# Performance work log

Hardware: AMD Instinct MI355X
Metric: run time of the kernel (lower is better)

## Reference

```python
import jax, jax.numpy as jnp
import numpy as np

B, T, C = 2, 2048, 2048
N_HEAD, N_KV_HEAD, HEAD_DIM = 16, 4, 128
N_REP = N_HEAD // N_KV_HEAD
EPS = 1e-05


def setup_inputs() -> dict:
    key = jax.random.key(0)
    ks = jax.random.split(key, 8)
    # rope freqs as cos/sin of theta_t,i = t / 10000^(2i/d)
    inv_freq = 1.0 / (10000.0 ** (np.arange(0, HEAD_DIM, 2, dtype=np.float32) / HEAD_DIM))
    ang = np.arange(T, dtype=np.float32)[:, None] * inv_freq[None, :]  # [T, HEAD_DIM//2]
    scale = 0.02
    return {
        "x": jax.random.normal(ks[0], (B, T, C), jnp.float32),
        "freqs_cos": jnp.asarray(np.cos(ang)),
        "freqs_sin": jnp.asarray(np.sin(ang)),
        "wq": jax.random.normal(ks[1], (C, N_HEAD * HEAD_DIM), jnp.float32) * scale,
        "wk": jax.random.normal(ks[2], (C, N_KV_HEAD * HEAD_DIM), jnp.float32) * scale,
        "wv": jax.random.normal(ks[3], (C, N_KV_HEAD * HEAD_DIM), jnp.float32) * scale,
        "wo": jax.random.normal(ks[4], (N_HEAD * HEAD_DIM, C), jnp.float32) * scale,
        "q_norm_w": jnp.ones((HEAD_DIM,), jnp.float32),
        "k_norm_w": jnp.ones((HEAD_DIM,), jnp.float32),
    }


def _rmsnorm(x, w):
    var = jnp.mean(jnp.square(x), axis=-1, keepdims=True)
    return x * jax.lax.rsqrt(var + EPS) * w


def _rope(x, cos, sin):
    # x: [B, T, H, D]; interpret last dim as interleaved (real, imag) pairs
    xr = x[..., 0::2]
    xi = x[..., 1::2]
    c = cos[None, :, None, :]
    s = sin[None, :, None, :]
    out_r = xr * c - xi * s
    out_i = xr * s + xi * c
    return jnp.stack([out_r, out_i], axis=-1).reshape(x.shape)


def reference(x, freqs_cos, freqs_sin, wq, wk, wv, wo, q_norm_w, k_norm_w):
    # QKV projections
    xq = (x @ wq).reshape(B, T, N_HEAD, HEAD_DIM)
    xk = (x @ wk).reshape(B, T, N_KV_HEAD, HEAD_DIM)
    xv = (x @ wv).reshape(B, T, N_KV_HEAD, HEAD_DIM)
    # optional q/k RMSNorm (use_qk_norm=True)
    xq = _rmsnorm(xq, q_norm_w)
    xk = _rmsnorm(xk, k_norm_w)
    # RoPE
    xq = _rope(xq, freqs_cos, freqs_sin)
    xk = _rope(xk, freqs_cos, freqs_sin)
    # GQA expand: each kv head repeated N_REP times contiguously
    xk = jnp.repeat(xk, N_REP, axis=2)  # [B, T, N_HEAD, D]
    xv = jnp.repeat(xv, N_REP, axis=2)
    # causal SDPA
    scores = jnp.einsum("bthd,bshd->bhts", xq, xk) / jnp.sqrt(jnp.float32(HEAD_DIM))
    causal = jnp.tril(jnp.ones((T, T), bool))
    scores = jnp.where(causal[None, None], scores, jnp.float32(-1e30))
    attn = jax.nn.softmax(scores, axis=-1)
    y = jnp.einsum("bhts,bshd->bthd", attn, xv).reshape(B, T, N_HEAD * HEAD_DIM)
    return y @ wo
```

## Files before the change

### kernel.cpp

```cpp
#include <hip/hip_runtime.h>
#include <hip/hip_bf16.h>

using u16 = unsigned short;
using u32 = unsigned int;

typedef short bf16x8 __attribute__((ext_vector_type(8)));
typedef float f32x4 __attribute__((ext_vector_type(4)));

#define AS1 __attribute__((address_space(1)))
#define AS3 __attribute__((address_space(3)))

__device__ __forceinline__ void gll16(const void* g, void* l) {
  __builtin_amdgcn_global_load_lds((const AS1 u32*)g, (AS3 u32*)l, 16, 0, 0);
}

__device__ __forceinline__ u16 f2bf(float x) {
  u32 u = __builtin_bit_cast(u32, x);
  u32 r = (u + 0x7fffu + ((u >> 16) & 1u)) >> 16;
  return (u16)r;
}
__device__ __forceinline__ u32 pk2(float lo, float hi) {
  return (u32)f2bf(lo) | ((u32)f2bf(hi) << 16);
}
__device__ __forceinline__ u16 f2bf_fast(float x) {
  __hip_bfloat16 h = __float2bfloat16(x);
  return __builtin_bit_cast(u16, h);
}

__device__ __forceinline__ void trans64(const float* __restrict__ in, u16* __restrict__ out,
                                        int R, int Cc, int bx, int by, float (*tl)[65]) {
  int c0 = bx * 64, r0 = by * 64, tid = threadIdx.x;
#pragma unroll
  for (int i = 0; i < 16; i++) {
    int idx = i * 256 + tid; int tr = idx >> 6, tc = idx & 63;
    tl[tr][tc] = in[(size_t)(r0 + tr) * Cc + c0 + tc];
  }
  __syncthreads();
#pragma unroll
  for (int i = 0; i < 16; i++) {
    int idx = i * 256 + tid; int tr = idx >> 6, tc = idx & 63;
    out[(size_t)(c0 + tr) * R + r0 + tc] = f2bf(tl[tc][tr]);
  }
}

__global__ void k_prep(const float* __restrict__ x, u16* __restrict__ xb,
                       const float* __restrict__ wq, u16* __restrict__ wqt,
                       const float* __restrict__ wk, const float* __restrict__ wv,
                       u16* __restrict__ wkvt,
                       const float* __restrict__ wo, u16* __restrict__ wot,
                       const float* __restrict__ fc, const float* __restrict__ fs,
                       float2* __restrict__ fcs) {
  __shared__ float tl[64][65];
  int gid = blockIdx.x;
  if (gid < 4096) {
    int i = gid * 256 + threadIdx.x;
    const float4* p = (const float4*)(x + (size_t)i * 8);
    float4 a = p[0], b = p[1];
    uint4 o;
    o.x = pk2(a.x, a.y); o.y = pk2(a.z, a.w);
    o.z = pk2(b.x, b.y); o.w = pk2(b.z, b.w);
    *(uint4*)(xb + (size_t)i * 8) = o;
  } else if (gid < 5120) {
    int t = gid - 4096; trans64(wq, wqt, 2048, 2048, t & 31, t >> 5, tl);
  } else if (gid < 5376) {
    int t = gid - 5120; trans64(wk, wkvt, 2048, 512, t & 7, t >> 3, tl);
  } else if (gid < 5632) {
    int t = gid - 5376; trans64(wv, wkvt + 512 * 2048, 2048, 512, t & 7, t >> 3, tl);
  } else if (gid < 6656) {
    int t = gid - 5632; trans64(wo, wot, 2048, 2048, t & 31, t >> 5, tl);
  } else {
    int base = (gid - 6656) * 2048 + threadIdx.x * 8;
#pragma unroll
    for (int j = 0; j < 8; j++) {
      int idx = base + j;
      fcs[idx] = make_float2(fc[idx], fs[idx]);
    }
  }
}

template <int MODE>
__global__ __launch_bounds__(256) void k_gemm(
    const u16* __restrict__ A, const u16* __restrict__ BT0, const u16* __restrict__ BT1,
    void* __restrict__ Cout, u16* __restrict__ Kout, u16* __restrict__ Vout, int K,
    const float* __restrict__ nwq, const float* __restrict__ nwk,
    const float2* __restrict__ fcs) {
  constexpr int NX = (MODE == 0) ? 16 : 24;
  constexpr int RBX = (MODE == 0) ? 8 : 12;
  __shared__ char lds[32768];
  char* As = lds; char* Bs = lds + 16384;
  int tid = threadIdx.x, w = tid >> 6, l = tid & 63, lg = l >> 4, ll = l & 15;
  int lid = blockIdx.y * NX + blockIdx.x;
  int xcd = lid & 7, r = lid >> 3;
  int colg = xcd & 1, rowg = xcd >> 1;
  int bxt = colg * RBX + r % RBX;
  int bm0 = (rowg * 8 + r / RBX) * 128;
  bool qpath = (MODE == 0) || (bxt < 16);
  const u16* BT = qpath ? BT0 : BT1;
  int bn0 = qpath ? bxt * 128 : (bxt - 16) * 128;
  int wr = w >> 1, wc = w & 1;
  f32x4 acc[4][4] = {};
  for (int k0 = 0; k0 < K; k0 += 64) {
#pragma unroll
    for (int i = 0; i < 4; i++) {
      int base = i * 256 + (w << 6);
      int p = base + l;
      int rr = p >> 3, kc = (p & 7) ^ (rr & 7);
      gll16(A + (size_t)(bm0 + rr) * K + k0 + kc * 8, As + base * 16);
      gll16(BT + (size_t)(bn0 + rr) * K + k0 + kc * 8, Bs + base * 16);
    }
    asm volatile("s_waitcnt vmcnt(0)" ::: "memory");
    __syncthreads();
#pragma unroll
    for (int ks = 0; ks < 2; ks++) {
      bf16x8 af[4], bfr[4];
#pragma unroll
      for (int m = 0; m < 4; m++) {
        int row = 64 * wr + 16 * m + ll;
        af[m] = *(const bf16x8*)(As + row * 128 + (((lg + 4 * ks) ^ (row & 7)) << 4));
      }
#pragma unroll
      for (int n = 0; n < 4; n++) {
        int row = 64 * wc + 16 * n + ll;
        bfr[n] = *(const bf16x8*)(Bs + row * 128 + (((lg + 4 * ks) ^ (row & 7)) << 4));
      }
#pragma unroll
      for (int m = 0; m < 4; m++)
#pragma unroll
        for (int n = 0; n < 4; n++)
          acc[m][n] = __builtin_amdgcn_mfma_f32_16x16x32_bf16(af[m], bfr[n], acc[m][n], 0, 0, 0);
    }
    __syncthreads();
  }

  if (MODE == 0) {
    float* C = (float*)Cout;
#pragma unroll
    for (int m = 0; m < 4; m++)
#pragma unroll
      for (int n = 0; n < 4; n++) {
        int row = bm0 + 64 * wr + 16 * m + 4 * lg;
        int col = bn0 + 64 * wc + 16 * n + ll;
        float* cp = C + (size_t)row * 2048 + col;
#pragma unroll
        for (int r2 = 0; r2 < 4; r2++) cp[(size_t)r2 * 2048] = acc[m][n][r2];
      }
    return;
  }

  if (qpath || bn0 < 512) {
    const float* nw = qpath ? nwq : nwk;
    u16* O = qpath ? (u16*)Cout : Kout;
    int ostride = qpath ? 2048 : 512;
    float outscale = qpath ? 0.12751744843f : 1.0f;
    float* ssum = (float*)lds;
    float ps[4][4];
#pragma unroll
    for (int m = 0; m < 4; m++)
#pragma unroll
      for (int r2 = 0; r2 < 4; r2++) {
        float p = 0.f;
#pragma unroll
        for (int n = 0; n < 4; n++) p += acc[m][n][r2] * acc[m][n][r2];
#pragma unroll
        for (int msk = 1; msk < 16; msk <<= 1) p += __shfl_xor(p, msk);
        ps[m][r2] = p;
      }
    if (ll == 0) {
#pragma unroll
      for (int m = 0; m < 4; m++)
#pragma unroll
        for (int r2 = 0; r2 < 4; r2++)
          ssum[wr * 128 + (16 * m + 4 * lg + r2) * 2 + wc] = ps[m][r2];
    }
    __syncthreads();
    float rs[4][4];
#pragma unroll
    for (int m = 0; m < 4; m++)
#pragma unroll
      for (int r2 = 0; r2 < 4; r2++) {
        int rowl = 16 * m + 4 * lg + r2;
        float tot = ssum[wr * 128 + rowl * 2] + ssum[wr * 128 + rowl * 2 + 1];
        rs[m][r2] = rsqrtf(tot * (1.0f / 128.0f) + 1e-5f) * outscale;
      }
#pragma unroll
    for (int m = 0; m < 4; m++)
#pragma unroll
      for (int n = 0; n < 4; n++) {
        int d = 64 * wc + 16 * n + ll;
        float wgt = nw[d];
        int i = d >> 1;
#pragma unroll
        for (int r2 = 0; r2 < 4; r2++) {
          int row = bm0 + 64 * wr + 16 * m + 4 * lg + r2;
          int t = row & 2047;
          float y = acc[m][n][r2] * rs[m][r2] * wgt;
          float p = __shfl_xor(y, 1);
          float2 cs = fcs[t * 64 + i];
          float o = (ll & 1) ? (p * cs.y + y * cs.x) : (y * cs.x - p * cs.y);
          O[(size_t)row * ostride + bn0 + d] = f2bf(o);
        }
      }
  } else {
    int b = bm0 >> 11, t0g = bm0 & 2047;
    int kvh = (bn0 - 512) >> 7;
    int bk = b * 4 + kvh;
#pragma unroll
    for (int m = 0; m < 4; m++)
#pragma unroll
      for (int n = 0; n < 4; n++) {
        int d = 64 * wc + 16 * n + ll;
        int tloc = 64 * wr + 16 * m + 4 * lg;
        u32 w0 = pk2(acc[m][n][0], acc[m][n][1]);
        u32 w1 = pk2(acc[m][n][2], acc[m][n][3]);
        int byte = (d * 256 + tloc * 2) ^ ((d & 7) << 4);
        *(uint2*)(lds + byte) = make_uint2(w0, w1);
      }
    __syncthreads();
    int tc = tid & 15, dbase = tid >> 4;
#pragma unroll
    for (int pass = 0; pass < 8; pass++) {
      int d = dbase + pass * 16;
      int byte = (d * 256 + tc * 16) ^ ((d & 7) << 4);
      uint4 v = *(const uint4*)(lds + byte);
      *(uint4*)(Vout + ((size_t)(bk * 128 + d)) * 2048 + t0g + tc * 8) = v;
    }
  }
}

__global__ __launch_bounds__(256, 4) void k_attn(
    const u16* __restrict__ Q, const u16* __restrict__ Kb,
    const u16* __restrict__ Vt, u16* __restrict__ Y) {
  __shared__ char lds[73728];
  char* Ps = lds + 65536;
  int tid = threadIdx.x, w = tid >> 6, l = tid & 63, lg = l >> 4, ll = l & 15;
  int fid = blockIdx.x;
  int g = fid & 7, rank = fid >> 3;
  int b = g >> 2, kvh = g & 3;
  int h = kvh * 4 + (rank & 3);
  int pairId = rank >> 2;
  const u16* Kbase = Kb + ((size_t)b * 2048) * 512 + kvh * 128;
  const u16* Vbase = Vt + ((size_t)(b * 4 + kvh) * 128) * 2048;

  const bf16x8 vones = {(short)0x3F80, (short)0x3F80, (short)0x3F80, (short)0x3F80,
                        (short)0x3F80, (short)0x3F80, (short)0x3F80, (short)0x3F80};

#pragma unroll 1
  for (int qi = 0; qi < 2; qi++) {
    int qb = qi ? (31 - pairId) : pairId;
    int q0 = qb * 64;
    bf16x8 qf[4];
    {
      int qrow = b * 2048 + q0 + 16 * w + ll;
      const u16* qp = Q + (size_t)qrow * 2048 + h * 128;
#pragma unroll
      for (int ks = 0; ks < 4; ks++) qf[ks] = *(const bf16x8*)(qp + ks * 32 + lg * 8);
    }
    f32x4 o[8] = {};
    f32x4 lacc = {};

    auto stage = [&](int bi, int k0) {
      char* Kd = lds + (bi ? 32768 : 0);
      char* Vd = lds + (bi ? 49152 : 16384);
#pragma unroll
      for (int i = 0; i < 4; i++) {
        int c = i * 256 + tid;
        int dst = (i * 256 + (w << 6)) * 16;
        int krow = c >> 4, ksrc = (c & 15) ^ (krow & 7);
        gll16(Kbase + (size_t)(k0 + krow) * 512 + ksrc * 8, Kd + dst);
        int vd = c >> 3, vsrc = (c & 7) ^ (vd & 7);
        gll16(Vbase + (size_t)vd * 2048 + k0 + vsrc * 8, Vd + dst);
      }
    };

    stage(0, 0);
    asm volatile("s_waitcnt vmcnt(0)" ::: "memory");
    __syncthreads();

    int cur = 0;
    for (int it = 0; it <= qb; ++it) {
      if (it < qb) stage(cur ^ 1, (it + 1) * 64);
      char* Ks = lds + (cur ? 32768 : 0);
      char* Vs = lds + (cur ? 49152 : 16384);
      f32x4 s[4] = {};
      __builtin_amdgcn_s_setprio(1);
#pragma unroll
      for (int ks = 0; ks < 4; ks++) {
#pragma unroll
        for (int n = 0; n < 4; n++) {
          int row = 16 * n + ll;
          bf16x8 kf = *(const bf16x8*)(Ks + ((row * 256 + (lg + 4 * ks) * 16) ^ ((row & 7) << 4)));
          s[n] = __builtin_amdgcn_mfma_f32_16x16x32_bf16(qf[ks], kf, s[n], 0, 0, 0);
        }
      }
      __builtin_amdgcn_s_setprio(0);
      if (it == qb) {
        int k0 = it * 64;
#pragma unroll
        for (int n = 0; n < 4; n++) {
          int kk = k0 + 16 * n + ll;
#pragma unroll
          for (int r = 0; r < 4; r++) {
            int qq = q0 + 16 * w + 4 * lg + r;
            if (kk > qq) s[n][r] = -1e30f;
          }
        }
      }
#pragma unroll
      for (int r = 0; r < 4; r++) {
        int prow = 4 * lg + r;
#pragma unroll
        for (int n = 0; n < 4; n++) {
          float e = exp2f(s[n][r]);
          int byte = (w << 11) + ((prow * 128 + (16 * n + ll) * 2) ^ ((prow & 7) << 4));
          *(u16*)(Ps + byte) = f2bf_fast(e);
        }
      }
      __builtin_amdgcn_s_setprio(1);
#pragma unroll
      for (int ks = 0; ks < 2; ks++) {
        bf16x8 pf = *(const bf16x8*)(Ps + (w << 11) + ((ll * 128 + (lg + 4 * ks) * 16) ^ ((ll & 7) << 4)));
        lacc = __builtin_amdgcn_mfma_f32_16x16x32_bf16(pf, vones, lacc, 0, 0, 0);
#pragma unroll
        for (int n = 0; n < 8; n++) {
          int row = 16 * n + ll;
          bf16x8 vf = *(const bf16x8*)(Vs + ((row * 128 + (lg + 4 * ks) * 16) ^ ((row & 7) << 4)));
          o[n] = __builtin_amdgcn_mfma_f32_16x16x32_bf16(pf, vf, o[n], 0, 0, 0);
        }
      }
      __builtin_amdgcn_s_setprio(0);
      asm volatile("s_waitcnt vmcnt(0)" ::: "memory");
      __syncthreads();
      cur ^= 1;
    }
    float rl[4];
#pragma unroll
    for (int r = 0; r < 4; r++) rl[r] = 1.0f / lacc[r];
#pragma unroll
    for (int n = 0; n < 8; n++) {
      int col = h * 128 + 16 * n + ll;
#pragma unroll
      for (int r = 0; r < 4; r++) {
        int trow = b * 2048 + q0 + 16 * w + 4 * lg + r;
        Y[(size_t)trow * 2048 + col] = f2bf_fast(o[n][r] * rl[r]);
      }
    }
  }
  (void)Vbase;
}

extern "C" void kernel_launch(void* const* d_in, const int* in_sizes, int n_in,
                              void* d_out, int out_size, void* d_ws, size_t ws_size,
                              hipStream_t stream) {
  const float* x   = (const float*)d_in[0];
  const float* fc  = (const float*)d_in[1];
  const float* fs  = (const float*)d_in[2];
  const float* wq  = (const float*)d_in[3];
  const float* wk  = (const float*)d_in[4];
  const float* wv  = (const float*)d_in[5];
  const float* wo  = (const float*)d_in[6];
  const float* qnw = (const float*)d_in[7];
  const float* knw = (const float*)d_in[8];
  float* out = (float*)d_out;

  const size_t MB = 1ull << 20;
  char* ws = (char*)d_ws;
  u16*    xb   = (u16*)(ws);
  u16*    wqt  = (u16*)(ws + 16 * MB);
  u16*    wkvt = (u16*)(ws + 24 * MB);
  u16*    wot  = (u16*)(ws + 28 * MB);
  u16*    Qb   = (u16*)(ws + 36 * MB);
  u16*    Kbq  = (u16*)(ws + 52 * MB);
  u16*    Vtg  = (u16*)(ws + 56 * MB);
  u16*    Yb   = (u16*)(ws + 60 * MB);
  float2* fcs  = (float2*)(ws + 76 * MB);

  hipLaunchKernelGGL(k_prep, dim3(6720), dim3(256), 0, stream,
                     x, xb, wq, wqt, wk, wv, wkvt, wo, wot, fc, fs, fcs);
  hipLaunchKernelGGL((k_gemm<3>), dim3(24, 32), dim3(256), 0, stream,
                     xb, wqt, wkvt, (void*)Qb, Kbq, Vtg, 2048,
                     qnw, knw, fcs);
  hipLaunchKernelGGL(k_attn, dim3(512), dim3(256), 0, stream, Qb, Kbq, Vtg, Yb);
  hipLaunchKernelGGL((k_gemm<0>), dim3(16, 32), dim3(256), 0, stream,
                     Yb, wot, (const u16*)nullptr, (void*)out, (u16*)nullptr, (u16*)nullptr, 2048,
                     nullptr, nullptr, nullptr);
}
```

Before: 216.0 us.

## Split QKV GEMM into triple-buffered 512-thread kernel with prefetch pipeline

```diff
diff --git a/kernel.cpp b/kernel.cpp
--- a/kernel.cpp
+++ b/kernel.cpp
@@ -84,8 +84,8 @@
     void* __restrict__ Cout, u16* __restrict__ Kout, u16* __restrict__ Vout, int K,
     const float* __restrict__ nwq, const float* __restrict__ nwk,
     const float2* __restrict__ fcs) {
-  constexpr int NX = (MODE == 0) ? 16 : 24;
-  constexpr int RBX = (MODE == 0) ? 8 : 12;
+  constexpr int NX = 16;
+  constexpr int RBX = 8;
   __shared__ char lds[32768];
   char* As = lds; char* Bs = lds + 16384;
   int tid = threadIdx.x, w = tid >> 6, l = tid & 63, lg = l >> 4, ll = l & 15;
@@ -94,9 +94,8 @@
   int colg = xcd & 1, rowg = xcd >> 1;
   int bxt = colg * RBX + r % RBX;
   int bm0 = (rowg * 8 + r / RBX) * 128;
-  bool qpath = (MODE == 0) || (bxt < 16);
-  const u16* BT = qpath ? BT0 : BT1;
-  int bn0 = qpath ? bxt * 128 : (bxt - 16) * 128;
+  const u16* BT = BT0;
+  int bn0 = bxt * 128;
   int wr = w >> 1, wc = w & 1;
   f32x4 acc[4][4] = {};
   for (int k0 = 0; k0 < K; k0 += 64) {
@@ -131,25 +130,96 @@
     }
     __syncthreads();
   }
-
-  if (MODE == 0) {
-    float* C = (float*)Cout;
-#pragma unroll
-    for (int m = 0; m < 4; m++)
-#pragma unroll
-      for (int n = 0; n < 4; n++) {
-        int row = bm0 + 64 * wr + 16 * m + 4 * lg;
-        int col = bn0 + 64 * wc + 16 * n + ll;
-        float* cp = C + (size_t)row * 2048 + col;
-#pragma unroll
-        for (int r2 = 0; r2 < 4; r2++) cp[(size_t)r2 * 2048] = acc[m][n][r2];
-      }
-    return;
+  float* C = (float*)Cout;
+#pragma unroll
+  for (int m = 0; m < 4; m++)
+#pragma unroll
+    for (int n = 0; n < 4; n++) {
+      int row = bm0 + 64 * wr + 16 * m + 4 * lg;
+      int col = bn0 + 64 * wc + 16 * n + ll;
+      float* cp = C + (size_t)row * 2048 + col;
+#pragma unroll
+      for (int r2 = 0; r2 < 4; r2++) cp[(size_t)r2 * 2048] = acc[m][n][r2];
+    }
+  (void)nwq; (void)nwk; (void)fcs; (void)Kout; (void)Vout;
+}
+
+__global__ __launch_bounds__(512, 2) void k_gemm_qkv(
+    const u16* __restrict__ A, const u16* __restrict__ BT0, const u16* __restrict__ BT1,
+    u16* __restrict__ Qout, u16* __restrict__ Kout, u16* __restrict__ Vout,
+    const float* __restrict__ nwq, const float* __restrict__ nwk,
+    const float2* __restrict__ fcs) {
+  __shared__ char lds[98304];
+  const int K = 2048;
+  int tid = threadIdx.x, w = tid >> 6, l = tid & 63, lg = l >> 4, ll = l & 15;
+  int wr = w >> 2, wc = w & 3;
+  int lid = blockIdx.y * 24 + blockIdx.x;
+  int xcd = lid & 7, r = lid >> 3;
+  int colg = xcd & 1, rowg = xcd >> 1;
+  int bxt = colg * 12 + r % 12;
+  int bm0 = (rowg * 8 + r / 12) * 128;
+  bool qpath = (bxt < 16);
+  const u16* BT = qpath ? BT0 : BT1;
+  int bn0 = qpath ? bxt * 128 : (bxt - 16) * 128;
+
+  auto stage = [&](int si, int kt) {
+    char* Sb = lds + si * 32768;
+    int k0 = kt * 64;
+#pragma unroll
+    for (int i = 0; i < 2; i++) {
+      int base = i * 512 + (w << 6) + ((tid >> 8) << 8);
+      base = i * 512 + (w << 6);
+      int c = base + l;
+      int row = c >> 3, kc = (c & 7) ^ (row & 7);
+      gll16(A + (size_t)(bm0 + row) * K + k0 + kc * 8, Sb + base * 16);
+      gll16(BT + (size_t)(bn0 + row) * K + k0 + kc * 8, Sb + 16384 + base * 16);
+    }
+  };
+
+  f32x4 acc[4][2] = {};
+  stage(0, 0); stage(1, 1);
+  asm volatile("s_waitcnt vmcnt(4)" ::: "memory");
+  __builtin_amdgcn_s_barrier();
+  __builtin_amdgcn_sched_barrier(0);
+
+  for (int kt = 0; kt < 32; ++kt) {
+    int cs = kt % 3;
+    if (kt + 2 < 32) stage((kt + 2) % 3, kt + 2);
+    char* As = lds + cs * 32768;
+    char* Bs = As + 16384;
+    __builtin_amdgcn_s_setprio(1);
+#pragma unroll
+    for (int ks = 0; ks < 2; ks++) {
+      bf16x8 af[4], bf[2];
+#pragma unroll
+      for (int m = 0; m < 4; m++) {
+        int row = 64 * wr + 16 * m + ll;
+        af[m] = *(const bf16x8*)(As + row * 128 + (((lg + 4 * ks) ^ (row & 7)) << 4));
+      }
+#pragma unroll
+      for (int n = 0; n < 2; n++) {
+        int row = 32 * wc + 16 * n + ll;
+        bf[n] = *(const bf16x8*)(Bs + row * 128 + (((lg + 4 * ks) ^ (row & 7)) << 4));
+      }
+#pragma unroll
+      for (int m = 0; m < 4; m++)
+#pragma unroll
+        for (int n = 0; n < 2; n++)
+          acc[m][n] = __builtin_amdgcn_mfma_f32_16x16x32_bf16(af[m], bf[n], acc[m][n], 0, 0, 0);
+    }
+    __builtin_amdgcn_s_setprio(0);
+    if (kt + 2 < 32) {
+      asm volatile("s_waitcnt vmcnt(4)" ::: "memory");
+    } else {
+      asm volatile("s_waitcnt vmcnt(0)" ::: "memory");
+    }
+    __builtin_amdgcn_s_barrier();
+    __builtin_amdgcn_sched_barrier(0);
   }
 
   if (qpath || bn0 < 512) {
     const float* nw = qpath ? nwq : nwk;
-    u16* O = qpath ? (u16*)Cout : Kout;
+    u16* O = qpath ? Qout : Kout;
     int ostride = qpath ? 2048 : 512;
     float outscale = qpath ? 0.12751744843f : 1.0f;
     float* ssum = (float*)lds;
@@ -160,7 +230,7 @@
       for (int r2 = 0; r2 < 4; r2++) {
         float p = 0.f;
 #pragma unroll
-        for (int n = 0; n < 4; n++) p += acc[m][n][r2] * acc[m][n][r2];
+        for (int n = 0; n < 2; n++) p += acc[m][n][r2] * acc[m][n][r2];
 #pragma unroll
         for (int msk = 1; msk < 16; msk <<= 1) p += __shfl_xor(p, msk);
         ps[m][r2] = p;
@@ -170,7 +240,7 @@
       for (int m = 0; m < 4; m++)
 #pragma unroll
         for (int r2 = 0; r2 < 4; r2++)
-          ssum[wr * 128 + (16 * m + 4 * lg + r2) * 2 + wc] = ps[m][r2];
+          ssum[wr * 256 + (16 * m + 4 * lg + r2) * 4 + wc] = ps[m][r2];
     }
     __syncthreads();
     float rs[4][4];
@@ -179,14 +249,16 @@
 #pragma unroll
       for (int r2 = 0; r2 < 4; r2++) {
         int rowl = 16 * m + 4 * lg + r2;
-        float tot = ssum[wr * 128 + rowl * 2] + ssum[wr * 128 + rowl * 2 + 1];
+        const float* sp = ssum + wr * 256 + rowl * 4;
+        float tot = sp[0] + sp[1] + sp[2] + sp[3];
         rs[m][r2] = rsqrtf(tot * (1.0f / 128.0f) + 1e-5f) * outscale;
       }
 #pragma unroll
     for (int m = 0; m < 4; m++)
 #pragma unroll
-      for (int n = 0; n < 4; n++) {
-        int d = 64 * wc + 16 * n + ll;
+      for (int n = 0; n < 2; n++) {
+        int col = bn0 + 32 * wc + 16 * n + ll;
+        int d = col & 127;
         float wgt = nw[d];
         int i = d >> 1;
 #pragma unroll
@@ -197,7 +269,7 @@
           float p = __shfl_xor(y, 1);
           float2 cs = fcs[t * 64 + i];
           float o = (ll & 1) ? (p * cs.y + y * cs.x) : (y * cs.x - p * cs.y);
-          O[(size_t)row * ostride + bn0 + d] = f2bf(o);
+          O[(size_t)row * ostride + col] = f2bf(o);
         }
       }
   } else {
@@ -207,8 +279,8 @@
 #pragma unroll
     for (int m = 0; m < 4; m++)
 #pragma unroll
-      for (int n = 0; n < 4; n++) {
-        int d = 64 * wc + 16 * n + ll;
+      for (int n = 0; n < 2; n++) {
+        int d = 32 * wc + 16 * n + ll;
         int tloc = 64 * wr + 16 * m + 4 * lg;
         u32 w0 = pk2(acc[m][n][0], acc[m][n][1]);
         u32 w1 = pk2(acc[m][n][2], acc[m][n][3]);
@@ -218,8 +290,8 @@
     __syncthreads();
     int tc = tid & 15, dbase = tid >> 4;
 #pragma unroll
-    for (int pass = 0; pass < 8; pass++) {
-      int d = dbase + pass * 16;
+    for (int pass = 0; pass < 4; pass++) {
+      int d = dbase + pass * 32;
       int byte = (d * 256 + tc * 16) ^ ((d & 7) << 4);
       uint4 v = *(const uint4*)(lds + byte);
       *(uint4*)(Vout + ((size_t)(bk * 128 + d)) * 2048 + t0g + tc * 8) = v;
@@ -376,9 +448,8 @@
 
   hipLaunchKernelGGL(k_prep, dim3(6720), dim3(256), 0, stream,
                      x, xb, wq, wqt, wk, wv, wkvt, wo, wot, fc, fs, fcs);
-  hipLaunchKernelGGL((k_gemm<3>), dim3(24, 32), dim3(256), 0, stream,
-                     xb, wqt, wkvt, (void*)Qb, Kbq, Vtg, 2048,
-                     qnw, knw, fcs);
+  hipLaunchKernelGGL(k_gemm_qkv, dim3(24, 32), dim3(512), 0, stream,
+                     xb, wqt, wkvt, Qb, Kbq, Vtg, qnw, knw, fcs);
   hipLaunchKernelGGL(k_attn, dim3(512), dim3(256), 0, stream, Qb, Kbq, Vtg, Yb);
   hipLaunchKernelGGL((k_gemm<0>), dim3(16, 32), dim3(256), 0, stream,
                      Yb, wot, (const u16*)nullptr, (void*)out, (u16*)nullptr, (u16*)nullptr, 2048,
```

New measurement: 207.5 us. 4.0% less time.
